# Kernel tuning notes

Measured on AMD Instinct MI355X. Metric: run time of the kernel, lower is better.

Reference implementation:

```python
import jax, jax.numpy as jnp
import numpy as np

DIM = 192
NH = 6
WZ = 8
SHIFT = WZ // 2  # shifted=True
SCALE = (DIM // NH) ** -0.5


def _rel_pos_idx(wz: int) -> np.ndarray:
    coords = np.stack(np.meshgrid(np.arange(wz), np.arange(wz), indexing='ij'))  # (2,wz,wz)
    flat = coords.reshape(2, -1)
    rel = flat[:, :, None] - flat[:, None, :]           # (2, N, N)
    rel = rel.transpose(1, 2, 0)                        # (N, N, 2)
    rel[:, :, 0] += wz - 1
    rel[:, :, 1] += wz - 1
    rel[:, :, 0] *= 2 * wz - 1
    return rel.sum(-1)                                  # (N, N) int


def setup_inputs() -> dict:
    key = jax.random.key(0)
    ks = jax.random.split(key, 6)
    B, C, H, W = 8, DIM, 224, 224
    x = jax.random.normal(ks[0], (B, C, H, W), dtype=jnp.float32)
    qkv_w = jax.random.normal(ks[1], (3 * DIM, DIM), dtype=jnp.float32) * 0.02
    qkv_b = jnp.zeros((3 * DIM,), dtype=jnp.float32)
    proj_w = jax.random.normal(ks[2], (DIM, DIM), dtype=jnp.float32) * 0.02
    proj_b = jnp.zeros((DIM,), dtype=jnp.float32)
    rel_pos_bias = jax.random.normal(ks[3], ((2 * WZ - 1) ** 2, NH), dtype=jnp.float32) * 0.02
    rel_pos_idx = jnp.asarray(_rel_pos_idx(WZ), dtype=jnp.int32)
    return {"x": x, "qkv_w": qkv_w, "qkv_b": qkv_b, "proj_w": proj_w,
            "proj_b": proj_b, "rel_pos_bias": rel_pos_bias, "rel_pos_idx": rel_pos_idx}


def reference(x, qkv_w, qkv_b, proj_w, proj_b, rel_pos_bias, rel_pos_idx):
    B, C, H, W = x.shape
    wz, nh, hd = WZ, NH, C // NH
    pad_h = (wz - H % wz) % wz
    pad_w = (wz - W % wz) % wz
    xh = jnp.transpose(x, (0, 2, 3, 1))                 # (B,H,W,C)
    if pad_h or pad_w:
        xh = jnp.pad(xh, ((0, 0), (0, pad_h), (0, pad_w), (0, 0)))
    Hp, Wp = xh.shape[1], xh.shape[2]
    xh = jnp.roll(xh, shift=(-SHIFT, -SHIFT), axis=(1, 2))
    # window partition: (B,Hp,Wp,C) -> (B*nW, N, C), N = wz*wz
    xh = xh.reshape(B, Hp // wz, wz, Wp // wz, wz, C)
    wins = jnp.transpose(xh, (0, 1, 3, 2, 4, 5)).reshape(-1, wz * wz, C)
    N = wz * wz
    qkv = wins @ qkv_w.T + qkv_b                        # (BnW, N, 3C)
    q, k, v = jnp.split(qkv, 3, axis=-1)
    def heads(t):
        return jnp.transpose(t.reshape(-1, N, nh, hd), (0, 2, 1, 3))  # (BnW,nh,N,hd)
    q, k, v = heads(q), heads(k), heads(v)
    bias = rel_pos_bias[rel_pos_idx.reshape(-1)].reshape(N, N, nh)
    bias = jnp.transpose(bias, (2, 0, 1))[None]         # (1,nh,N,N)
    attn = jnp.einsum('whnd,whmd->whnm', q, k) * SCALE + bias
    attn = jax.nn.softmax(attn, axis=-1)
    out = jnp.einsum('whnm,whmd->whnd', attn, v)        # (BnW,nh,N,hd)
    out = jnp.transpose(out, (0, 2, 1, 3)).reshape(-1, N, C)
    out = out @ proj_w.T + proj_b
    # window reverse
    out = out.reshape(B, Hp // wz, Wp // wz, wz, wz, C)
    out = jnp.transpose(out, (0, 1, 3, 2, 4, 5)).reshape(B, Hp, Wp, C)
    out = jnp.roll(out, shift=(SHIFT, SHIFT), axis=(1, 2))
    out = out[:, :H, :W, :]
    return jnp.transpose(out, (0, 3, 1, 2))             # (B,C,H,W)
```

## Files before the change

### kernel.cpp

```cpp
#include <hip/hip_runtime.h>
#include <hip/hip_bf16.h>
#include <stdint.h>

typedef unsigned short u16;
typedef short v8s __attribute__((ext_vector_type(8)));
typedef float v4f __attribute__((ext_vector_type(4)));
typedef uint32_t v2u __attribute__((ext_vector_type(2)));

#define DIM 192
#define NH 6
#define IMG 224
#define NWIN 28
#define NB 8
#define SCALE 0.17677669529663687f
#define AO_STR 200

#define SWZ(tok) ((((tok) & 7) ^ ((tok) >> 3)) << 3)

__device__ __forceinline__ u16 f2bf(float f) {
    union { __hip_bfloat16 b; u16 u; } c; c.b = __float2bfloat16(f); return c.u;
}
__device__ __forceinline__ uint32_t pk2(float lo, float hi) {
    union { __hip_bfloat162 b; uint32_t u; } c;
    c.b = __float22bfloat162_rn(make_float2(lo, hi));
    return c.u;
}

__global__ void prep_kernel(const float* __restrict__ qkv_w,
                            const float* __restrict__ qkv_b,
                            const float* __restrict__ proj_w,
                            const float* __restrict__ rel_bias,
                            const int* __restrict__ rel_idx,
                            u16* __restrict__ qw, u16* __restrict__ pw,
                            float* __restrict__ qb2, float* __restrict__ biasT) {
    int i = blockIdx.x * 256 + threadIdx.x;
    if (i < 3*DIM*DIM) {
        float s = (i < DIM*DIM) ? SCALE : 1.f;
        qw[i] = f2bf(qkv_w[i] * s);
    }
    if (i < DIM*DIM) pw[i] = f2bf(proj_w[i]);
    if (i < 3*DIM)   qb2[i] = qkv_b[i] * (i < DIM ? SCALE : 1.f);
    if (i < NH*64*64) {
        int h   = i >> 12;
        int qk2 = i & 4095;
        biasT[i] = rel_bias[rel_idx[qk2]*NH + h];
    }
}

__global__ __launch_bounds__(768, 3) void winattn_kernel(
    const float* __restrict__ x,
    const float* __restrict__ proj_b,
    const u16* __restrict__ qw,
    const u16* __restrict__ pw,
    const float* __restrict__ qb2,
    const float* __restrict__ biasT,
    float* __restrict__ out)
{
    __shared__ __align__(16) u16 bufX[2][64 * DIM];
    __shared__ __align__(16) u16 bufO[2][64 * AO_STR];

    const int tid  = threadIdx.x;
    const int wv   = tid >> 6;
    const int h    = wv >> 1;
    const int win  = wv & 1;
    const int lane = tid & 63;
    const int l15  = lane & 15;
    const int g    = lane >> 4;

    const int b  = blockIdx.x & 7;
    const int rm = blockIdx.x >> 3;

    const float* xb = x   + (size_t)b * DIM*IMG*IMG;
    float*       ob = out + (size_t)b * DIM*IMG*IMG;

    {
        const int gwin = (tid >= 384) ? 1 : 0;
        const int tl   = tid - gwin*384;
        const int widx = rm*2 + gwin;
        const int gwi  = widx / NWIN, gwj = widx - gwi*NWIN;
        const int qq   = tl & 15;
        const int trow = qq >> 1;
        const int tcol = (qq & 1) * 4;
        const int t0   = trow*8 + tcol;
        const int c0   = tl >> 4;
        int ghh = gwi*8 + trow + 4; if (ghh >= IMG) ghh -= IMG;
        int gww = gwj*8 + tcol + 4; if (gww >= IMG) gww -= IMG;
        const size_t pixoff = (size_t)ghh*IMG + gww;

        v4f buf[8];
        #pragma unroll
        for (int it = 0; it < 8; ++it)
            buf[it] = *(const v4f*)(xb + (size_t)(c0 + it*24)*(IMG*IMG) + pixoff);
        u16* bX = bufX[gwin];
        #pragma unroll
        for (int it = 0; it < 8; ++it) {
            int c = c0 + it*24;
            #pragma unroll
            for (int i = 0; i < 4; ++i) {
                int tok = t0 + i;
                bX[tok*DIM + (c ^ SWZ(tok))] = f2bf(buf[it][i]);
            }
        }
    }
    __syncthreads();

    const int widx = rm*2 + win;
    const int wi = widx / NWIN, wj = widx - wi*NWIN;
    u16* bX = bufX[win];
    u16* bO = bufO[win];

    uint32_t vd[4][2][2];
    {
        v4f vacc[4][2];
        #pragma unroll
        for (int mt = 0; mt < 4; ++mt)
            #pragma unroll
            for (int ntl = 0; ntl < 2; ++ntl)
                vacc[mt][ntl] = (v4f){0.f,0.f,0.f,0.f};
        #pragma unroll
        for (int kk = 0; kk < 6; ++kk) {
            v8s xfr[4];
            #pragma unroll
            for (int mt = 0; mt < 4; ++mt) {
                int tok = mt*16 + l15;
                xfr[mt] = *(const v8s*)&bX[tok*DIM + ((kk*32 + g*8) ^ SWZ(tok))];
            }
            v8s wvf[2];
            #pragma unroll
            for (int ntl = 0; ntl < 2; ++ntl)
                wvf[ntl] = *(const v8s*)(qw + (size_t)(2*DIM + h*32 + ntl*16 + l15)*DIM + kk*32 + g*8);
            __builtin_amdgcn_s_setprio(1);
            #pragma unroll
            for (int ntl = 0; ntl < 2; ++ntl)
                #pragma unroll
                for (int mt = 0; mt < 4; ++mt)
                    vacc[mt][ntl] = __builtin_amdgcn_mfma_f32_16x16x32_bf16(xfr[mt], wvf[ntl], vacc[mt][ntl], 0, 0, 0);
            __builtin_amdgcn_s_setprio(0);
        }
        #pragma unroll
        for (int ntl = 0; ntl < 2; ++ntl) {
            const float bv = qb2[2*DIM + h*32 + ntl*16 + l15];
            #pragma unroll
            for (int mt = 0; mt < 4; ++mt) {
                vd[mt][ntl][0] = pk2(vacc[mt][ntl][0]+bv, vacc[mt][ntl][1]+bv);
                vd[mt][ntl][1] = pk2(vacc[mt][ntl][2]+bv, vacc[mt][ntl][3]+bv);
            }
        }
    }

    v8s qfr[4], kfr[4];
    {
        v4f qacc[2][4], kacc[2][4];
        #pragma unroll
        for (int ntl = 0; ntl < 2; ++ntl)
            #pragma unroll
            for (int qt = 0; qt < 4; ++qt) {
                qacc[ntl][qt] = (v4f){0.f,0.f,0.f,0.f};
                kacc[ntl][qt] = (v4f){0.f,0.f,0.f,0.f};
            }
        #pragma unroll
        for (int kk = 0; kk < 6; ++kk) {
            v8s xfr[4];
            #pragma unroll
            for (int qt = 0; qt < 4; ++qt) {
                int tok = qt*16 + l15;
                xfr[qt] = *(const v8s*)&bX[tok*DIM + ((kk*32 + g*8) ^ SWZ(tok))];
            }
            v8s wq[2], wk[2];
            #pragma unroll
            for (int ntl = 0; ntl < 2; ++ntl) {
                wq[ntl] = *(const v8s*)(qw + (size_t)(h*32 + ntl*16 + l15)*DIM + kk*32 + g*8);
                wk[ntl] = *(const v8s*)(qw + (size_t)(DIM + h*32 + ntl*16 + l15)*DIM + kk*32 + g*8);
            }
            __builtin_amdgcn_s_setprio(1);
            #pragma unroll
            for (int ntl = 0; ntl < 2; ++ntl)
                #pragma unroll
                for (int qt = 0; qt < 4; ++qt) {
                    qacc[ntl][qt] = __builtin_amdgcn_mfma_f32_16x16x32_bf16(wq[ntl], xfr[qt], qacc[ntl][qt], 0, 0, 0);
                    kacc[ntl][qt] = __builtin_amdgcn_mfma_f32_16x16x32_bf16(wk[ntl], xfr[qt], kacc[ntl][qt], 0, 0, 0);
                }
            __builtin_amdgcn_s_setprio(0);
        }
        v4f bqv[2], bkv[2];
        #pragma unroll
        for (int ntl = 0; ntl < 2; ++ntl) {
            bqv[ntl] = *(const v4f*)&qb2[h*32 + ntl*16 + 4*g];
            bkv[ntl] = *(const v4f*)&qb2[DIM + h*32 + ntl*16 + 4*g];
        }
        #pragma unroll
        for (int qt = 0; qt < 4; ++qt) {
            union { v8s v; uint32_t d[4]; } uq, uk;
            uq.d[0] = pk2(qacc[0][qt][0]+bqv[0][0], qacc[0][qt][1]+bqv[0][1]);
            uq.d[1] = pk2(qacc[0][qt][2]+bqv[0][2], qacc[0][qt][3]+bqv[0][3]);
            uq.d[2] = pk2(qacc[1][qt][0]+bqv[1][0], qacc[1][qt][1]+bqv[1][1]);
            uq.d[3] = pk2(qacc[1][qt][2]+bqv[1][2], qacc[1][qt][3]+bqv[1][3]);
            uk.d[0] = pk2(kacc[0][qt][0]+bkv[0][0], kacc[0][qt][1]+bkv[0][1]);
            uk.d[1] = pk2(kacc[0][qt][2]+bkv[0][2], kacc[0][qt][3]+bkv[0][3]);
            uk.d[2] = pk2(kacc[1][qt][0]+bkv[1][0], kacc[1][qt][1]+bkv[1][1]);
            uk.d[3] = pk2(kacc[1][qt][2]+bkv[1][2], kacc[1][qt][3]+bkv[1][3]);
            qfr[qt] = uq.v;
            kfr[qt] = uk.v;
        }
    }

    uint32_t pd[2][4][4];
    const float* bt = biasT + h*4096;
    #pragma unroll
    for (int qt = 0; qt < 4; ++qt) {
        v4f bb[4];
        #pragma unroll
        for (int kt = 0; kt < 4; ++kt)
            bb[kt] = *(const v4f*)&bt[(qt*16 + l15)*64 + kt*16 + 4*g];
        v4f sq[4];
        __builtin_amdgcn_s_setprio(1);
        #pragma unroll
        for (int kt = 0; kt < 4; ++kt)
            sq[kt] = __builtin_amdgcn_mfma_f32_16x16x32_bf16(kfr[kt], qfr[qt],
                         (v4f){0.f,0.f,0.f,0.f}, 0, 0, 0);
        __builtin_amdgcn_s_setprio(0);
        #pragma unroll
        for (int kt = 0; kt < 4; ++kt) sq[kt] += bb[kt];
        float mx = sq[0][0];
        #pragma unroll
        for (int kt = 0; kt < 4; ++kt)
            #pragma unroll
            for (int r = 0; r < 4; ++r) mx = fmaxf(mx, sq[kt][r]);
        mx = fmaxf(mx, __shfl_xor(mx, 16));
        mx = fmaxf(mx, __shfl_xor(mx, 32));
        float sum = 0.f;
        #pragma unroll
        for (int kt = 0; kt < 4; ++kt)
            #pragma unroll
            for (int r = 0; r < 4; ++r) {
                float e = __expf(sq[kt][r] - mx);
                sq[kt][r] = e; sum += e;
            }
        sum += __shfl_xor(sum, 16);
        sum += __shfl_xor(sum, 32);
        float inv = 1.f / sum;
        #pragma unroll
        for (int kt = 0; kt < 4; ++kt)
            #pragma unroll
            for (int r = 0; r < 4; ++r) sq[kt][r] *= inv;

        pd[0][qt][0] = pk2(sq[0][0], sq[0][1]);
        pd[0][qt][1] = pk2(sq[0][2], sq[0][3]);
        pd[0][qt][2] = pk2(sq[1][0], sq[1][1]);
        pd[0][qt][3] = pk2(sq[1][2], sq[1][3]);
        pd[1][qt][0] = pk2(sq[2][0], sq[2][1]);
        pd[1][qt][1] = pk2(sq[2][2], sq[2][3]);
        pd[1][qt][2] = pk2(sq[3][0], sq[3][1]);
        pd[1][qt][3] = pk2(sq[3][2], sq[3][3]);
    }

    v4f oT[2][4];
    #pragma unroll
    for (int ntl = 0; ntl < 2; ++ntl)
        #pragma unroll
        for (int qt = 0; qt < 4; ++qt)
            oT[ntl][qt] = (v4f){0.f,0.f,0.f,0.f};
    #pragma unroll
    for (int kk = 0; kk < 2; ++kk) {
        v8s vfr[2];
        #pragma unroll
        for (int ntl = 0; ntl < 2; ++ntl) {
            union { v8s v; uint32_t d[4]; } uu;
            uu.d[0] = vd[2*kk  ][ntl][0]; uu.d[1] = vd[2*kk  ][ntl][1];
            uu.d[2] = vd[2*kk+1][ntl][0]; uu.d[3] = vd[2*kk+1][ntl][1];
            vfr[ntl] = uu.v;
        }
        __builtin_amdgcn_s_setprio(1);
        #pragma unroll
        for (int qt = 0; qt < 4; ++qt) {
            union { v8s v; uint32_t d[4]; } p;
            p.d[0] = pd[kk][qt][0]; p.d[1] = pd[kk][qt][1];
            p.d[2] = pd[kk][qt][2]; p.d[3] = pd[kk][qt][3];
            #pragma unroll
            for (int ntl = 0; ntl < 2; ++ntl)
                oT[ntl][qt] = __builtin_amdgcn_mfma_f32_16x16x32_bf16(vfr[ntl], p.v, oT[ntl][qt], 0, 0, 0);
        }
        __builtin_amdgcn_s_setprio(0);
    }

    #pragma unroll
    for (int qt = 0; qt < 4; ++qt)
        #pragma unroll
        for (int ntl = 0; ntl < 2; ++ntl) {
            v2u o;
            o.x = pk2(oT[ntl][qt][0], oT[ntl][qt][1]);
            o.y = pk2(oT[ntl][qt][2], oT[ntl][qt][3]);
            *(v2u*)&bO[(qt*16 + l15)*AO_STR + h*32 + ntl*16 + 4*g] = o;
        }
    __syncthreads();

    v4f pacc[2][4];
    #pragma unroll
    for (int ntl = 0; ntl < 2; ++ntl)
        #pragma unroll
        for (int qt = 0; qt < 4; ++qt)
            pacc[ntl][qt] = (v4f){0.f,0.f,0.f,0.f};
    #pragma unroll
    for (int kk = 0; kk < 6; ++kk) {
        v8s aofr[4];
        #pragma unroll
        for (int qt = 0; qt < 4; ++qt)
            aofr[qt] = *(const v8s*)&bO[(qt*16 + l15)*AO_STR + kk*32 + g*8];
        v8s pwfr[2];
        #pragma unroll
        for (int ntl = 0; ntl < 2; ++ntl)
            pwfr[ntl] = *(const v8s*)(pw + (size_t)(h*32 + ntl*16 + l15)*DIM + kk*32 + g*8);
        __builtin_amdgcn_s_setprio(1);
        #pragma unroll
        for (int ntl = 0; ntl < 2; ++ntl)
            #pragma unroll
            for (int qt = 0; qt < 4; ++qt)
                pacc[ntl][qt] = __builtin_amdgcn_mfma_f32_16x16x32_bf16(pwfr[ntl], aofr[qt], pacc[ntl][qt], 0, 0, 0);
        __builtin_amdgcn_s_setprio(0);
    }
    float pb[2][4];
    #pragma unroll
    for (int ntl = 0; ntl < 2; ++ntl) {
        v4f pbv = *(const v4f*)&proj_b[h*32 + ntl*16 + 4*g];
        #pragma unroll
        for (int r = 0; r < 4; ++r) pb[ntl][r] = pbv[r];
    }

    #pragma unroll
    for (int qt = 0; qt < 4; ++qt) {
        const int strow = 2*qt + (l15 >> 3);
        const int stcol = l15 & 7;
        int hh = wi*8 + strow + 4; if (hh >= IMG) hh -= IMG;
        int ww = wj*8 + stcol + 4; if (ww >= IMG) ww -= IMG;
        const size_t pix = (size_t)hh*IMG + ww;
        #pragma unroll
        for (int ntl = 0; ntl < 2; ++ntl)
            #pragma unroll
            for (int r = 0; r < 4; ++r) {
                const int c = h*32 + ntl*16 + 4*g + r;
                ob[(size_t)c*(IMG*IMG) + pix] = pacc[ntl][qt][r] + pb[ntl][r];
            }
    }
}

extern "C" void kernel_launch(void* const* d_in, const int* in_sizes, int n_in,
                              void* d_out, int out_size, void* d_ws, size_t ws_size,
                              hipStream_t stream) {
    const float* x        = (const float*)d_in[0];
    const float* qkv_w    = (const float*)d_in[1];
    const float* qkv_b    = (const float*)d_in[2];
    const float* proj_w   = (const float*)d_in[3];
    const float* proj_b   = (const float*)d_in[4];
    const float* rel_bias = (const float*)d_in[5];
    const int*   rel_idx  = (const int*)d_in[6];

    u16*   qw_bf  = (u16*)d_ws;
    u16*   pw_bf  = (u16*)((char*)d_ws + 221184);
    float* qb2    = (float*)((char*)d_ws + 294912);
    float* biasT  = (float*)((char*)d_ws + 297216);
    float* out    = (float*)d_out;

    hipLaunchKernelGGL(prep_kernel, dim3(432), dim3(256), 0, stream,
                       qkv_w, qkv_b, proj_w, rel_bias, rel_idx, qw_bf, pw_bf, qb2, biasT);
    hipLaunchKernelGGL(winattn_kernel, dim3(NB * (NWIN*NWIN/2)), dim3(768), 0, stream,
                       x, proj_b, qw_bf, pw_bf, qb2, biasT, out);
}
```

Baseline: 495.0 us.

## Make window-attention kernel persistent with double-buffered prefetch of next window pair

The kernel now runs a fixed grid of 768 blocks that loop over window pairs. Each block issues the global gather for its next pair into registers while the projection GEMM of the current pair runs, then commits it to a second shared-memory X buffer. This hides global load latency and cuts block launch overhead. The cost is more LDS per block (doubled X buffer) and higher register pressure from the held gather values, which may lower occupancy; the P@V loop was also restructured to pack V fragments directly.

```diff
diff --git a/kernel.cpp b/kernel.cpp
--- a/kernel.cpp
+++ b/kernel.cpp
@@ -12,6 +12,8 @@
 #define IMG 224
 #define NWIN 28
 #define NB 8
+#define NPAIRS (NB*NWIN*NWIN/2)
+#define GRID 768
 #define SCALE 0.17677669529663687f
 #define AO_STR 200
 
@@ -56,7 +58,7 @@
     const float* __restrict__ biasT,
     float* __restrict__ out)
 {
-    __shared__ __align__(16) u16 bufX[2][64 * DIM];
+    __shared__ __align__(16) u16 bufX[2][2][64 * DIM];
     __shared__ __align__(16) u16 bufO[2][64 * AO_STR];
 
     const int tid  = threadIdx.x;
@@ -67,279 +69,280 @@
     const int l15  = lane & 15;
     const int g    = lane >> 4;
 
-    const int b  = blockIdx.x & 7;
-    const int rm = blockIdx.x >> 3;
+    const int bid = blockIdx.x;
+    const int b   = bid & 7;
 
     const float* xb = x   + (size_t)b * DIM*IMG*IMG;
     float*       ob = out + (size_t)b * DIM*IMG*IMG;
 
-    {
-        const int gwin = (tid >= 384) ? 1 : 0;
-        const int tl   = tid - gwin*384;
+    const int gwin  = (tid >= 384) ? 1 : 0;
+    const int tl    = tid - gwin*384;
+    const int gq    = tl & 15;
+    const int gtrow = gq >> 1;
+    const int gtcol = (gq & 1) * 4;
+    const int gt0   = gtrow*8 + gtcol;
+    const int gc0   = tl >> 4;
+
+    v4f gbuf[8];
+    auto issue_gather = [&](int rm) {
         const int widx = rm*2 + gwin;
-        const int gwi  = widx / NWIN, gwj = widx - gwi*NWIN;
-        const int qq   = tl & 15;
-        const int trow = qq >> 1;
-        const int tcol = (qq & 1) * 4;
-        const int t0   = trow*8 + tcol;
-        const int c0   = tl >> 4;
-        int ghh = gwi*8 + trow + 4; if (ghh >= IMG) ghh -= IMG;
-        int gww = gwj*8 + tcol + 4; if (gww >= IMG) gww -= IMG;
+        const int gwi = widx / NWIN, gwj = widx - gwi*NWIN;
+        int ghh = gwi*8 + gtrow + 4; if (ghh >= IMG) ghh -= IMG;
+        int gww = gwj*8 + gtcol + 4; if (gww >= IMG) gww -= IMG;
         const size_t pixoff = (size_t)ghh*IMG + gww;
-
-        v4f buf[8];
         #pragma unroll
         for (int it = 0; it < 8; ++it)
-            buf[it] = *(const v4f*)(xb + (size_t)(c0 + it*24)*(IMG*IMG) + pixoff);
-        u16* bX = bufX[gwin];
+            gbuf[it] = *(const v4f*)(xb + (size_t)(gc0 + it*24)*(IMG*IMG) + pixoff);
+    };
+    auto commit_gather = [&](u16* bX) {
         #pragma unroll
         for (int it = 0; it < 8; ++it) {
-            int c = c0 + it*24;
-            #pragma unroll
-            for (int i = 0; i < 4; ++i) {
-                int tok = t0 + i;
-                bX[tok*DIM + (c ^ SWZ(tok))] = f2bf(buf[it][i]);
-            }
-        }
-    }
+            int c = gc0 + it*24;
+            #pragma unroll
+            for (int i2 = 0; i2 < 4; ++i2) {
+                int tok = gt0 + i2;
+                bX[tok*DIM + (c ^ SWZ(tok))] = f2bf(gbuf[it][i2]);
+            }
+        }
+    };
+
+    issue_gather(bid >> 3);
+    commit_gather(&bufX[0][gwin][0]);
     __syncthreads();
 
-    const int widx = rm*2 + win;
-    const int wi = widx / NWIN, wj = widx - wi*NWIN;
-    u16* bX = bufX[win];
-    u16* bO = bufO[win];
-
-    uint32_t vd[4][2][2];
-    {
-        v4f vacc[4][2];
-        #pragma unroll
-        for (int mt = 0; mt < 4; ++mt)
+    int k = 0;
+    #pragma unroll 1
+    for (int P = bid; P < NPAIRS; P += GRID, ++k) {
+        const int par  = k & 1;
+        const int rm   = P >> 3;
+        const int widx = rm*2 + win;
+        const int wi = widx / NWIN, wj = widx - wi*NWIN;
+        u16* bX = &bufX[par][win][0];
+        u16* bO = &bufO[win][0];
+        const bool hasNext = (P + GRID) < NPAIRS;
+
+        v8s vfr[2][2];
+        {
+            v4f vacc[4][2];
+            #pragma unroll
+            for (int mt = 0; mt < 4; ++mt)
+                #pragma unroll
+                for (int ntl = 0; ntl < 2; ++ntl)
+                    vacc[mt][ntl] = (v4f){0.f,0.f,0.f,0.f};
+            #pragma unroll
+            for (int kk = 0; kk < 6; ++kk) {
+                v8s xfr[4];
+                #pragma unroll
+                for (int mt = 0; mt < 4; ++mt) {
+                    int tok = mt*16 + l15;
+                    xfr[mt] = *(const v8s*)&bX[tok*DIM + ((kk*32 + g*8) ^ SWZ(tok))];
+                }
+                v8s wvf[2];
+                #pragma unroll
+                for (int ntl = 0; ntl < 2; ++ntl)
+                    wvf[ntl] = *(const v8s*)(qw + (size_t)(2*DIM + h*32 + ntl*16 + l15)*DIM + kk*32 + g*8);
+                __builtin_amdgcn_s_setprio(1);
+                #pragma unroll
+                for (int ntl = 0; ntl < 2; ++ntl)
+                    #pragma unroll
+                    for (int mt = 0; mt < 4; ++mt)
+                        vacc[mt][ntl] = __builtin_amdgcn_mfma_f32_16x16x32_bf16(xfr[mt], wvf[ntl], vacc[mt][ntl], 0, 0, 0);
+                __builtin_amdgcn_s_setprio(0);
+            }
+            #pragma unroll
+            for (int ntl = 0; ntl < 2; ++ntl) {
+                const float bv = qb2[2*DIM + h*32 + ntl*16 + l15];
+                #pragma unroll
+                for (int kk = 0; kk < 2; ++kk) {
+                    union { v8s v; uint32_t d[4]; } uu;
+                    uu.d[0] = pk2(vacc[2*kk  ][ntl][0]+bv, vacc[2*kk  ][ntl][1]+bv);
+                    uu.d[1] = pk2(vacc[2*kk  ][ntl][2]+bv, vacc[2*kk  ][ntl][3]+bv);
+                    uu.d[2] = pk2(vacc[2*kk+1][ntl][0]+bv, vacc[2*kk+1][ntl][1]+bv);
+                    uu.d[3] = pk2(vacc[2*kk+1][ntl][2]+bv, vacc[2*kk+1][ntl][3]+bv);
+                    vfr[kk][ntl] = uu.v;
+                }
+            }
+        }
+
+        v8s qfr[4], kfr[4];
+        {
+            v4f qacc[2][4], kacc[2][4];
             #pragma unroll
             for (int ntl = 0; ntl < 2; ++ntl)
-                vacc[mt][ntl] = (v4f){0.f,0.f,0.f,0.f};
+                #pragma unroll
+                for (int qt = 0; qt < 4; ++qt) {
+                    qacc[ntl][qt] = (v4f){0.f,0.f,0.f,0.f};
+                    kacc[ntl][qt] = (v4f){0.f,0.f,0.f,0.f};
+                }
+            #pragma unroll
+            for (int kk = 0; kk < 6; ++kk) {
+                v8s xfr[4];
+                #pragma unroll
+                for (int qt = 0; qt < 4; ++qt) {
+                    int tok = qt*16 + l15;
+                    xfr[qt] = *(const v8s*)&bX[tok*DIM + ((kk*32 + g*8) ^ SWZ(tok))];
+                }
+                v8s wq[2], wk[2];
+                #pragma unroll
+                for (int ntl = 0; ntl < 2; ++ntl) {
+                    wq[ntl] = *(const v8s*)(qw + (size_t)(h*32 + ntl*16 + l15)*DIM + kk*32 + g*8);
+                    wk[ntl] = *(const v8s*)(qw + (size_t)(DIM + h*32 + ntl*16 + l15)*DIM + kk*32 + g*8);
+                }
+                __builtin_amdgcn_s_setprio(1);
+                #pragma unroll
+                for (int ntl = 0; ntl < 2; ++ntl)
+                    #pragma unroll
+                    for (int qt = 0; qt < 4; ++qt) {
+                        qacc[ntl][qt] = __builtin_amdgcn_mfma_f32_16x16x32_bf16(wq[ntl], xfr[qt], qacc[ntl][qt], 0, 0, 0);
+                        kacc[ntl][qt] = __builtin_amdgcn_mfma_f32_16x16x32_bf16(wk[ntl], xfr[qt], kacc[ntl][qt], 0, 0, 0);
+                    }
+                __builtin_amdgcn_s_setprio(0);
+            }
+            v4f bqv[2], bkv[2];
+            #pragma unroll
+            for (int ntl = 0; ntl < 2; ++ntl) {
+                bqv[ntl] = *(const v4f*)&qb2[h*32 + ntl*16 + 4*g];
+                bkv[ntl] = *(const v4f*)&qb2[DIM + h*32 + ntl*16 + 4*g];
+            }
+            #pragma unroll
+            for (int qt = 0; qt < 4; ++qt) {
+                union { v8s v; uint32_t d[4]; } uq, uk;
+                uq.d[0] = pk2(qacc[0][qt][0]+bqv[0][0], qacc[0][qt][1]+bqv[0][1]);
+                uq.d[1] = pk2(qacc[0][qt][2]+bqv[0][2], qacc[0][qt][3]+bqv[0][3]);
+                uq.d[2] = pk2(qacc[1][qt][0]+bqv[1][0], qacc[1][qt][1]+bqv[1][1]);
+                uq.d[3] = pk2(qacc[1][qt][2]+bqv[1][2], qacc[1][qt][3]+bqv[1][3]);
+                uk.d[0] = pk2(kacc[0][qt][0]+bkv[0][0], kacc[0][qt][1]+bkv[0][1]);
+                uk.d[1] = pk2(kacc[0][qt][2]+bkv[0][2], kacc[0][qt][3]+bkv[0][3]);
+                uk.d[2] = pk2(kacc[1][qt][0]+bkv[1][0], kacc[1][qt][1]+bkv[1][1]);
+                uk.d[3] = pk2(kacc[1][qt][2]+bkv[1][2], kacc[1][qt][3]+bkv[1][3]);
+                qfr[qt] = uq.v;
+                kfr[qt] = uk.v;
+            }
+        }
+
+        v4f oT[2][4];
+        #pragma unroll
+        for (int ntl = 0; ntl < 2; ++ntl)
+            #pragma unroll
+            for (int qt = 0; qt < 4; ++qt)
+                oT[ntl][qt] = (v4f){0.f,0.f,0.f,0.f};
+        const float* bt = biasT + h*4096;
+        #pragma unroll
+        for (int qt = 0; qt < 4; ++qt) {
+            v4f bb[4];
+            #pragma unroll
+            for (int kt = 0; kt < 4; ++kt)
+                bb[kt] = *(const v4f*)&bt[(qt*16 + l15)*64 + kt*16 + 4*g];
+            v4f sq[4];
+            __builtin_amdgcn_s_setprio(1);
+            #pragma unroll
+            for (int kt = 0; kt < 4; ++kt)
+                sq[kt] = __builtin_amdgcn_mfma_f32_16x16x32_bf16(kfr[kt], qfr[qt],
+                             (v4f){0.f,0.f,0.f,0.f}, 0, 0, 0);
+            __builtin_amdgcn_s_setprio(0);
+            #pragma unroll
+            for (int kt = 0; kt < 4; ++kt) sq[kt] += bb[kt];
+            float mx = sq[0][0];
+            #pragma unroll
+            for (int kt = 0; kt < 4; ++kt)
+                #pragma unroll
+                for (int r = 0; r < 4; ++r) mx = fmaxf(mx, sq[kt][r]);
+            mx = fmaxf(mx, __shfl_xor(mx, 16));
+            mx = fmaxf(mx, __shfl_xor(mx, 32));
+            float sum = 0.f;
+            #pragma unroll
+            for (int kt = 0; kt < 4; ++kt)
+                #pragma unroll
+                for (int r = 0; r < 4; ++r) {
+                    float e = __expf(sq[kt][r] - mx);
+                    sq[kt][r] = e; sum += e;
+                }
+            sum += __shfl_xor(sum, 16);
+            sum += __shfl_xor(sum, 32);
+            float inv = 1.f / sum;
+            #pragma unroll
+            for (int kt = 0; kt < 4; ++kt)
+                #pragma unroll
+                for (int r = 0; r < 4; ++r) sq[kt][r] *= inv;
+
+            union { v8s v; uint32_t d[4]; } p0, p1;
+            p0.d[0] = pk2(sq[0][0], sq[0][1]); p0.d[1] = pk2(sq[0][2], sq[0][3]);
+            p0.d[2] = pk2(sq[1][0], sq[1][1]); p0.d[3] = pk2(sq[1][2], sq[1][3]);
+            p1.d[0] = pk2(sq[2][0], sq[2][1]); p1.d[1] = pk2(sq[2][2], sq[2][3]);
+            p1.d[2] = pk2(sq[3][0], sq[3][1]); p1.d[3] = pk2(sq[3][2], sq[3][3]);
+            __builtin_amdgcn_s_setprio(1);
+            #pragma unroll
+            for (int ntl = 0; ntl < 2; ++ntl) {
+                oT[ntl][qt] = __builtin_amdgcn_mfma_f32_16x16x32_bf16(vfr[0][ntl], p0.v, oT[ntl][qt], 0, 0, 0);
+                oT[ntl][qt] = __builtin_amdgcn_mfma_f32_16x16x32_bf16(vfr[1][ntl], p1.v, oT[ntl][qt], 0, 0, 0);
+            }
+            __builtin_amdgcn_s_setprio(0);
+        }
+
+        #pragma unroll
+        for (int qt = 0; qt < 4; ++qt)
+            #pragma unroll
+            for (int ntl = 0; ntl < 2; ++ntl) {
+                v2u o;
+                o.x = pk2(oT[ntl][qt][0], oT[ntl][qt][1]);
+                o.y = pk2(oT[ntl][qt][2], oT[ntl][qt][3]);
+                *(v2u*)&bO[(qt*16 + l15)*AO_STR + h*32 + ntl*16 + 4*g] = o;
+            }
+        __syncthreads();
+
+        if (hasNext) issue_gather((P + GRID) >> 3);
+
+        v4f pacc[2][4];
+        #pragma unroll
+        for (int ntl = 0; ntl < 2; ++ntl)
+            #pragma unroll
+            for (int qt = 0; qt < 4; ++qt)
+                pacc[ntl][qt] = (v4f){0.f,0.f,0.f,0.f};
         #pragma unroll
         for (int kk = 0; kk < 6; ++kk) {
-            v8s xfr[4];
-            #pragma unroll
-            for (int mt = 0; mt < 4; ++mt) {
-                int tok = mt*16 + l15;
-                xfr[mt] = *(const v8s*)&bX[tok*DIM + ((kk*32 + g*8) ^ SWZ(tok))];
-            }
-            v8s wvf[2];
+            v8s aofr[4];
+            #pragma unroll
+            for (int qt = 0; qt < 4; ++qt)
+                aofr[qt] = *(const v8s*)&bO[(qt*16 + l15)*AO_STR + kk*32 + g*8];
+            v8s pwfr[2];
             #pragma unroll
             for (int ntl = 0; ntl < 2; ++ntl)
-                wvf[ntl] = *(const v8s*)(qw + (size_t)(2*DIM + h*32 + ntl*16 + l15)*DIM + kk*32 + g*8);
+                pwfr[ntl] = *(const v8s*)(pw + (size_t)(h*32 + ntl*16 + l15)*DIM + kk*32 + g*8);
             __builtin_amdgcn_s_setprio(1);
             #pragma unroll
             for (int ntl = 0; ntl < 2; ++ntl)
                 #pragma unroll
-                for (int mt = 0; mt < 4; ++mt)
-                    vacc[mt][ntl] = __builtin_amdgcn_mfma_f32_16x16x32_bf16(xfr[mt], wvf[ntl], vacc[mt][ntl], 0, 0, 0);
+                for (int qt = 0; qt < 4; ++qt)
+                    pacc[ntl][qt] = __builtin_amdgcn_mfma_f32_16x16x32_bf16(pwfr[ntl], aofr[qt], pacc[ntl][qt], 0, 0, 0);
             __builtin_amdgcn_s_setprio(0);
         }
+        float pb[2][4];
         #pragma unroll
         for (int ntl = 0; ntl < 2; ++ntl) {
-            const float bv = qb2[2*DIM + h*32 + ntl*16 + l15];
-            #pragma unroll
-            for (int mt = 0; mt < 4; ++mt) {
-                vd[mt][ntl][0] = pk2(vacc[mt][ntl][0]+bv, vacc[mt][ntl][1]+bv);
-                vd[mt][ntl][1] = pk2(vacc[mt][ntl][2]+bv, vacc[mt][ntl][3]+bv);
-            }
-        }
-    }
-
-    v8s qfr[4], kfr[4];
-    {
-        v4f qacc[2][4], kacc[2][4];
-        #pragma unroll
-        for (int ntl = 0; ntl < 2; ++ntl)
-            #pragma unroll
-            for (int qt = 0; qt < 4; ++qt) {
-                qacc[ntl][qt] = (v4f){0.f,0.f,0.f,0.f};
-                kacc[ntl][qt] = (v4f){0.f,0.f,0.f,0.f};
-            }
-        #pragma unroll
-        for (int kk = 0; kk < 6; ++kk) {
-            v8s xfr[4];
-            #pragma unroll
-            for (int qt = 0; qt < 4; ++qt) {
-                int tok = qt*16 + l15;
-                xfr[qt] = *(const v8s*)&bX[tok*DIM + ((kk*32 + g*8) ^ SWZ(tok))];
-            }
-            v8s wq[2], wk[2];
-            #pragma unroll
-            for (int ntl = 0; ntl < 2; ++ntl) {
-                wq[ntl] = *(const v8s*)(qw + (size_t)(h*32 + ntl*16 + l15)*DIM + kk*32 + g*8);
-                wk[ntl] = *(const v8s*)(qw + (size_t)(DIM + h*32 + ntl*16 + l15)*DIM + kk*32 + g*8);
-            }
-            __builtin_amdgcn_s_setprio(1);
+            v4f pbv = *(const v4f*)&proj_b[h*32 + ntl*16 + 4*g];
+            #pragma unroll
+            for (int r = 0; r < 4; ++r) pb[ntl][r] = pbv[r];
+        }
+        #pragma unroll
+        for (int qt = 0; qt < 4; ++qt) {
+            const int strow = 2*qt + (l15 >> 3);
+            const int stcol = l15 & 7;
+            int hh = wi*8 + strow + 4; if (hh >= IMG) hh -= IMG;
+            int ww = wj*8 + stcol + 4; if (ww >= IMG) ww -= IMG;
+            const size_t pix = (size_t)hh*IMG + ww;
             #pragma unroll
             for (int ntl = 0; ntl < 2; ++ntl)
                 #pragma unroll
-                for (int qt = 0; qt < 4; ++qt) {
-                    qacc[ntl][qt] = __builtin_amdgcn_mfma_f32_16x16x32_bf16(wq[ntl], xfr[qt], qacc[ntl][qt], 0, 0, 0);
-                    kacc[ntl][qt] = __builtin_amdgcn_mfma_f32_16x16x32_bf16(wk[ntl], xfr[qt], kacc[ntl][qt], 0, 0, 0);
-                }
-            __builtin_amdgcn_s_setprio(0);
-        }
-        v4f bqv[2], bkv[2];
-        #pragma unroll
-        for (int ntl = 0; ntl < 2; ++ntl) {
-            bqv[ntl] = *(const v4f*)&qb2[h*32 + ntl*16 + 4*g];
-            bkv[ntl] = *(const v4f*)&qb2[DIM + h*32 + ntl*16 + 4*g];
-        }
-        #pragma unroll
-        for (int qt = 0; qt < 4; ++qt) {
-            union { v8s v; uint32_t d[4]; } uq, uk;
-            uq.d[0] = pk2(qacc[0][qt][0]+bqv[0][0], qacc[0][qt][1]+bqv[0][1]);
-            uq.d[1] = pk2(qacc[0][qt][2]+bqv[0][2], qacc[0][qt][3]+bqv[0][3]);
-            uq.d[2] = pk2(qacc[1][qt][0]+bqv[1][0], qacc[1][qt][1]+bqv[1][1]);
-            uq.d[3] = pk2(qacc[1][qt][2]+bqv[1][2], qacc[1][qt][3]+bqv[1][3]);
-            uk.d[0] = pk2(kacc[0][qt][0]+bkv[0][0], kacc[0][qt][1]+bkv[0][1]);
-            uk.d[1] = pk2(kacc[0][qt][2]+bkv[0][2], kacc[0][qt][3]+bkv[0][3]);
-            uk.d[2] = pk2(kacc[1][qt][0]+bkv[1][0], kacc[1][qt][1]+bkv[1][1]);
-            uk.d[3] = pk2(kacc[1][qt][2]+bkv[1][2], kacc[1][qt][3]+bkv[1][3]);
-            qfr[qt] = uq.v;
-            kfr[qt] = uk.v;
-        }
-    }
-
-    uint32_t pd[2][4][4];
-    const float* bt = biasT + h*4096;
-    #pragma unroll
-    for (int qt = 0; qt < 4; ++qt) {
-        v4f bb[4];
-        #pragma unroll
-        for (int kt = 0; kt < 4; ++kt)
-            bb[kt] = *(const v4f*)&bt[(qt*16 + l15)*64 + kt*16 + 4*g];
-        v4f sq[4];
-        __builtin_amdgcn_s_setprio(1);
-        #pragma unroll
-        for (int kt = 0; kt < 4; ++kt)
-            sq[kt] = __builtin_amdgcn_mfma_f32_16x16x32_bf16(kfr[kt], qfr[qt],
-                         (v4f){0.f,0.f,0.f,0.f}, 0, 0, 0);
-        __builtin_amdgcn_s_setprio(0);
-        #pragma unroll
-        for (int kt = 0; kt < 4; ++kt) sq[kt] += bb[kt];
-        float mx = sq[0][0];
-        #pragma unroll
-        for (int kt = 0; kt < 4; ++kt)
-            #pragma unroll
-            for (int r = 0; r < 4; ++r) mx = fmaxf(mx, sq[kt][r]);
-        mx = fmaxf(mx, __shfl_xor(mx, 16));
-        mx = fmaxf(mx, __shfl_xor(mx, 32));
-        float sum = 0.f;
-        #pragma unroll
-        for (int kt = 0; kt < 4; ++kt)
-            #pragma unroll
-            for (int r = 0; r < 4; ++r) {
-                float e = __expf(sq[kt][r] - mx);
-                sq[kt][r] = e; sum += e;
-            }
-        sum += __shfl_xor(sum, 16);
-        sum += __shfl_xor(sum, 32);
-        float inv = 1.f / sum;
-        #pragma unroll
-        for (int kt = 0; kt < 4; ++kt)
-            #pragma unroll
-            for (int r = 0; r < 4; ++r) sq[kt][r] *= inv;
-
-        pd[0][qt][0] = pk2(sq[0][0], sq[0][1]);
-        pd[0][qt][1] = pk2(sq[0][2], sq[0][3]);
-        pd[0][qt][2] = pk2(sq[1][0], sq[1][1]);
-        pd[0][qt][3] = pk2(sq[1][2], sq[1][3]);
-        pd[1][qt][0] = pk2(sq[2][0], sq[2][1]);
-        pd[1][qt][1] = pk2(sq[2][2], sq[2][3]);
-        pd[1][qt][2] = pk2(sq[3][0], sq[3][1]);
-        pd[1][qt][3] = pk2(sq[3][2], sq[3][3]);
-    }
-
-    v4f oT[2][4];
-    #pragma unroll
-    for (int ntl = 0; ntl < 2; ++ntl)
-        #pragma unroll
-        for (int qt = 0; qt < 4; ++qt)
-            oT[ntl][qt] = (v4f){0.f,0.f,0.f,0.f};
-    #pragma unroll
-    for (int kk = 0; kk < 2; ++kk) {
-        v8s vfr[2];
-        #pragma unroll
-        for (int ntl = 0; ntl < 2; ++ntl) {
-            union { v8s v; uint32_t d[4]; } uu;
-            uu.d[0] = vd[2*kk  ][ntl][0]; uu.d[1] = vd[2*kk  ][ntl][1];
-            uu.d[2] = vd[2*kk+1][ntl][0]; uu.d[3] = vd[2*kk+1][ntl][1];
-            vfr[ntl] = uu.v;
-        }
-        __builtin_amdgcn_s_setprio(1);
-        #pragma unroll
-        for (int qt = 0; qt < 4; ++qt) {
-            union { v8s v; uint32_t d[4]; } p;
-            p.d[0] = pd[kk][qt][0]; p.d[1] = pd[kk][qt][1];
-            p.d[2] = pd[kk][qt][2]; p.d[3] = pd[kk][qt][3];
-            #pragma unroll
-            for (int ntl = 0; ntl < 2; ++ntl)
-                oT[ntl][qt] = __builtin_amdgcn_mfma_f32_16x16x32_bf16(vfr[ntl], p.v, oT[ntl][qt], 0, 0, 0);
-        }
-        __builtin_amdgcn_s_setprio(0);
-    }
-
-    #pragma unroll
-    for (int qt = 0; qt < 4; ++qt)
-        #pragma unroll
-        for (int ntl = 0; ntl < 2; ++ntl) {
-            v2u o;
-            o.x = pk2(oT[ntl][qt][0], oT[ntl][qt][1]);
-            o.y = pk2(oT[ntl][qt][2], oT[ntl][qt][3]);
-            *(v2u*)&bO[(qt*16 + l15)*AO_STR + h*32 + ntl*16 + 4*g] = o;
-        }
-    __syncthreads();
-
-    v4f pacc[2][4];
-    #pragma unroll
-    for (int ntl = 0; ntl < 2; ++ntl)
-        #pragma unroll
-        for (int qt = 0; qt < 4; ++qt)
-            pacc[ntl][qt] = (v4f){0.f,0.f,0.f,0.f};
-    #pragma unroll
-    for (int kk = 0; kk < 6; ++kk) {
-        v8s aofr[4];
-        #pragma unroll
-        for (int qt = 0; qt < 4; ++qt)
-            aofr[qt] = *(const v8s*)&bO[(qt*16 + l15)*AO_STR + kk*32 + g*8];
-        v8s pwfr[2];
-        #pragma unroll
-        for (int ntl = 0; ntl < 2; ++ntl)
-            pwfr[ntl] = *(const v8s*)(pw + (size_t)(h*32 + ntl*16 + l15)*DIM + kk*32 + g*8);
-        __builtin_amdgcn_s_setprio(1);
-        #pragma unroll
-        for (int ntl = 0; ntl < 2; ++ntl)
-            #pragma unroll
-            for (int qt = 0; qt < 4; ++qt)
-                pacc[ntl][qt] = __builtin_amdgcn_mfma_f32_16x16x32_bf16(pwfr[ntl], aofr[qt], pacc[ntl][qt], 0, 0, 0);
-        __builtin_amdgcn_s_setprio(0);
-    }
-    float pb[2][4];
-    #pragma unroll
-    for (int ntl = 0; ntl < 2; ++ntl) {
-        v4f pbv = *(const v4f*)&proj_b[h*32 + ntl*16 + 4*g];
-        #pragma unroll
-        for (int r = 0; r < 4; ++r) pb[ntl][r] = pbv[r];
-    }
-
-    #pragma unroll
-    for (int qt = 0; qt < 4; ++qt) {
-        const int strow = 2*qt + (l15 >> 3);
-        const int stcol = l15 & 7;
-        int hh = wi*8 + strow + 4; if (hh >= IMG) hh -= IMG;
-        int ww = wj*8 + stcol + 4; if (ww >= IMG) ww -= IMG;
-        const size_t pix = (size_t)hh*IMG + ww;
-        #pragma unroll
-        for (int ntl = 0; ntl < 2; ++ntl)
-            #pragma unroll
-            for (int r = 0; r < 4; ++r) {
-                const int c = h*32 + ntl*16 + 4*g + r;
-                ob[(size_t)c*(IMG*IMG) + pix] = pacc[ntl][qt][r] + pb[ntl][r];
-            }
+                for (int r = 0; r < 4; ++r) {
+                    const int c = h*32 + ntl*16 + 4*g + r;
+                    ob[(size_t)c*(IMG*IMG) + pix] = pacc[ntl][qt][r] + pb[ntl][r];
+                }
+        }
+
+        if (hasNext) {
+            commit_gather(&bufX[par ^ 1][gwin][0]);
+            __syncthreads();
+        }
     }
 }
 
@@ -362,6 +365,6 @@
 
     hipLaunchKernelGGL(prep_kernel, dim3(432), dim3(256), 0, stream,
                        qkv_w, qkv_b, proj_w, rel_bias, rel_idx, qw_bf, pw_bf, qb2, biasT);
-    hipLaunchKernelGGL(winattn_kernel, dim3(NB * (NWIN*NWIN/2)), dim3(768), 0, stream,
+    hipLaunchKernelGGL(winattn_kernel, dim3(GRID), dim3(768), 0, stream,
                        x, proj_b, qw_bf, pw_bf, qb2, biasT, out);
 }
```

Result: slower. 1.432 ms (+189.3%).
